# Optimization experiments

Measured on AMD Instinct MI355X. Metric: run time of the kernel, lower is better.

Reference implementation:

```python
import jax, jax.numpy as jnp
import numpy as np

D_MODEL = 5120
NUM_HEADS = 128
HEAD_DIM = D_MODEL // NUM_HEADS  # 40
LATENT = 1536


def setup_inputs() -> dict:
    key = jax.random.key(0)
    ks = jax.random.split(key, 9)
    B, S = 2, 1024
    scale = 0.02
    return {
        "x": jax.random.normal(ks[0], (B, S, D_MODEL), dtype=jnp.float32),
        "Wq": jax.random.normal(ks[1], (D_MODEL, D_MODEL), dtype=jnp.float32) * scale,
        "bq": jnp.zeros((D_MODEL,), dtype=jnp.float32),
        "Wc": jax.random.normal(ks[2], (D_MODEL, LATENT), dtype=jnp.float32) * scale,
        "bc": jnp.zeros((LATENT,), dtype=jnp.float32),
        "Wk": jax.random.normal(ks[3], (LATENT, D_MODEL), dtype=jnp.float32) * scale,
        "bk": jnp.zeros((D_MODEL,), dtype=jnp.float32),
        "Wv": jax.random.normal(ks[4], (LATENT, D_MODEL), dtype=jnp.float32) * scale,
        "bv": jnp.zeros((D_MODEL,), dtype=jnp.float32),
    }


def reference(x, Wq, bq, Wc, bc, Wk, bk, Wv, bv):
    B, S, _ = x.shape
    H, Dh = NUM_HEADS, HEAD_DIM
    # projections
    q = x @ Wq + bq                     # [B,S,D]
    kv_latent = x @ Wc + bc             # [B,S,L]
    k = kv_latent @ Wk + bk             # [B,S,D]
    v = kv_latent @ Wv + bv             # [B,S,D]
    # split heads -> [B,H,S,Dh]
    q = q.reshape(B, S, H, Dh).transpose(0, 2, 1, 3)
    k = k.reshape(B, S, H, Dh).transpose(0, 2, 1, 3)
    v = v.reshape(B, S, H, Dh).transpose(0, 2, 1, 3)
    scores = jnp.einsum("bhqd,bhkd->bhqk", q, k) / jnp.sqrt(jnp.float32(Dh))
    attn = jax.nn.softmax(scores, axis=-1)
    out = jnp.einsum("bhqk,bhkd->bhqd", attn, v)  # [B,H,S,Dh]
    return out.transpose(0, 2, 1, 3).reshape(B, S, H * Dh)
```

## Files before the change

kernel.cpp:

```cpp
#include <hip/hip_runtime.h>
#include <hip/hip_bf16.h>

typedef __attribute__((ext_vector_type(8))) __bf16 bf16x8;
typedef __attribute__((ext_vector_type(4))) __bf16 bf16x4;
typedef __attribute__((ext_vector_type(4))) float f32x4;

#define MFMA16(a, b, c) __builtin_amdgcn_mfma_f32_16x16x32_bf16((a), (b), (c), 0, 0, 0)

#if __has_builtin(__builtin_amdgcn_exp2f)
#define EXP2F(x) __builtin_amdgcn_exp2f(x)
#else
#define EXP2F(x) exp2f(x)
#endif

#define GLDS16(g, l)                                                             \
    __builtin_amdgcn_global_load_lds((const __attribute__((address_space(1))) void*)(g), \
                                     (__attribute__((address_space(3))) void*)(l), 16, 0, 0)

#define BARRIER()                          \
    do {                                   \
        asm volatile("" ::: "memory");     \
        __builtin_amdgcn_s_barrier();      \
        asm volatile("" ::: "memory");     \
    } while (0)

#define WAIT_LGKM0() asm volatile("s_waitcnt lgkmcnt(0)" ::: "memory")
#define VM6 asm volatile("s_waitcnt vmcnt(6)" ::: "memory")
#define VM8 asm volatile("s_waitcnt vmcnt(8)" ::: "memory")
#define VM0 asm volatile("s_waitcnt vmcnt(0)" ::: "memory")
#define VMNONE ((void)0)
#define KEEP(x) x
#define DROP(x)

static __device__ __forceinline__ unsigned short cvt_bf(float f) {
    return __builtin_bit_cast(unsigned short, (__bf16)f);
}

static __device__ __forceinline__ bf16x8 bf8_zero() {
    uint4 z = make_uint4(0, 0, 0, 0);
    return __builtin_bit_cast(bf16x8, z);
}

__global__ __launch_bounds__(256) void prep(const float* __restrict__ X,
                                            const float* __restrict__ Wq,
                                            const float* __restrict__ Wc,
                                            const float* __restrict__ Wk,
                                            const float* __restrict__ Wv,
                                            unsigned short* __restrict__ Xb,
                                            unsigned short* __restrict__ dqc,
                                            unsigned short* __restrict__ dkv) {
    const int D = 5120, L = 1536;
    int b = blockIdx.x, t = threadIdx.x;
    if (b < 5120) {
        int i = (b * 256 + t) * 8;
        float4 f0 = *(const float4*)(X + i);
        float4 f1 = *(const float4*)(X + i + 4);
        unsigned short o[8];
        o[0] = cvt_bf(f0.x); o[1] = cvt_bf(f0.y); o[2] = cvt_bf(f0.z); o[3] = cvt_bf(f0.w);
        o[4] = cvt_bf(f1.x); o[5] = cvt_bf(f1.y); o[6] = cvt_bf(f1.z); o[7] = cvt_bf(f1.w);
        *(uint4*)(Xb + i) = *(const uint4*)o;
        return;
    }
    int b2 = b - 5120;
    const float* W;
    unsigned short* WT;
    int K, N;
    if (b2 < 6400) { W = Wq; WT = dqc; K = D; N = D; }
    else if (b2 < 8320) { b2 -= 6400; W = Wc; WT = dqc + (size_t)D * D; K = D; N = L; }
    else if (b2 < 10240) { b2 -= 8320; W = Wk; WT = dkv; K = L; N = D; }
    else { b2 -= 10240; W = Wv; WT = dkv + (size_t)D * L; K = L; N = D; }
    int nx = N / 64;
    int n0 = (b2 % nx) * 64, k0 = (b2 / nx) * 64;

    __shared__ unsigned short tile[64][65];
    int c4 = (t & 15) * 4, r16 = t >> 4;
#pragma unroll
    for (int it = 0; it < 4; ++it) {
        int r = r16 + it * 16;
        float4 f = *(const float4*)&W[(size_t)(k0 + r) * N + n0 + c4];
        tile[r][c4 + 0] = cvt_bf(f.x);
        tile[r][c4 + 1] = cvt_bf(f.y);
        tile[r][c4 + 2] = cvt_bf(f.z);
        tile[r][c4 + 3] = cvt_bf(f.w);
    }
    __syncthreads();
    int n = t >> 2, kc = (t & 3) * 16;
    unsigned short o[16];
#pragma unroll
    for (int j = 0; j < 16; ++j) o[j] = tile[kc + j][n];
    unsigned short* dst = &WT[(size_t)(n0 + n) * K + k0 + kc];
    *(uint4*)dst = *(const uint4*)o;
    *(uint4*)(dst + 8) = *(const uint4*)(o + 8);
}

#define STAGE_A(S, H, KT)                                                              \
    do {                                                                               \
        GLDS16(aS[H][0] + (size_t)(KT) * 64, &Abuf[S][(H) * 8192 + wid * 512]);        \
        GLDS16(aS[H][1] + (size_t)(KT) * 64, &Abuf[S][(H) * 8192 + 4096 + wid * 512]); \
    } while (0)
#define STAGE_B(S, H, KT)                                                              \
    do {                                                                               \
        GLDS16(bS[H][0] + (size_t)(KT) * 64, &Bbuf[S][(H) * 8192 + wid * 512]);        \
        GLDS16(bS[H][1] + (size_t)(KT) * 64, &Bbuf[S][(H) * 8192 + 4096 + wid * 512]); \
    } while (0)

#define LDA_HALF(S, QM)                                                                   \
    do {                                                                                  \
        _Pragma("unroll") for (int mi = 0; mi < 4; ++mi)                                  \
            _Pragma("unroll") for (int kh = 0; kh < 2; ++kh)                              \
                af[mi][kh] =                                                              \
                    *(const bf16x8*)&Abuf[S][((QM) * 8192 + aoff + mi * 1024) ^ (kh * 32)]; \
    } while (0)
#define LDB_HALF(S, QN, BF)                                                               \
    do {                                                                                  \
        _Pragma("unroll") for (int ni = 0; ni < 2; ++ni)                                  \
            _Pragma("unroll") for (int kh = 0; kh < 2; ++kh)                              \
                BF[ni][kh] =                                                              \
                    *(const bf16x8*)&Bbuf[S][((QN) * 8192 + boff + ni * 1024) ^ (kh * 32)]; \
    } while (0)

#define MMAQ(QM, QN, BF)                                                                \
    do {                                                                                \
        _Pragma("unroll") for (int mi = 0; mi < 4; ++mi)                                \
            _Pragma("unroll") for (int ni = 0; ni < 2; ++ni)                            \
                _Pragma("unroll") for (int kh = 0; kh < 2; ++kh)                        \
                    acc[(QM) * 4 + mi][(QN) * 2 + ni] =                                 \
                        MFMA16(af[mi][kh], BF[ni][kh], acc[(QM) * 4 + mi][(QN) * 2 + ni]); \
    } while (0)

#define KTILE_V2(S, T, STG1, STG2, VMOP, RDNEXT)       \
    {                                                  \
        const int s_ = (S);                            \
        LDB_HALF(s_, 1, bf1);                          \
        STG1(STAGE_B(s_ ^ 1, 0, (T) + 1);)             \
        __builtin_amdgcn_s_setprio(1);                 \
        MMAQ(0, 0, bf0);                               \
        __builtin_amdgcn_s_setprio(0);                 \
        WAIT_LGKM0();                                  \
        BARRIER();                                     \
        STG2(STAGE_A(s_, 0, (T) + 2);                  \
             STAGE_B(s_, 1, (T) + 2);)                 \
        __builtin_amdgcn_s_setprio(1);                 \
        MMAQ(0, 1, bf1);                               \
        __builtin_amdgcn_s_setprio(0);                 \
        LDA_HALF(s_, 1);                               \
        __builtin_amdgcn_s_setprio(1);                 \
        MMAQ(1, 1, bf1);                               \
        __builtin_amdgcn_s_setprio(0);                 \
        WAIT_LGKM0();                                  \
        BARRIER();                                     \
        STG2(STAGE_A(s_, 1, (T) + 2);)                 \
        __builtin_amdgcn_s_setprio(1);                 \
        MMAQ(1, 0, bf0);                               \
        __builtin_amdgcn_s_setprio(0);                 \
        VMOP;                                          \
        BARRIER();                                     \
        RDNEXT(LDA_HALF(s_ ^ 1, 0); LDB_HALF(s_ ^ 1, 0, bf0);) \
    }

__global__ __launch_bounds__(512, 2) void gemm256(const unsigned short* __restrict__ A, int lda,
                                                  const unsigned short* __restrict__ BT, int ldb,
                                                  const float* __restrict__ bias0,
                                                  const float* __restrict__ bias1, int nsplit,
                                                  unsigned short* __restrict__ C, int ldc,
                                                  int K, float s0, float s1, int gx) {
    __shared__ __align__(16) unsigned short Abuf[2][16384];
    __shared__ __align__(16) unsigned short Bbuf[2][16384];

    int nwg = gridDim.x, orig = blockIdx.x;
    int cpx = nwg >> 3;
    int wgid = (orig & 7) * cpx + (orig >> 3);
    int tm = wgid / gx, tn = wgid % gx;
    int m0 = tm * 256, n0 = tn * 256;

    int tid = threadIdx.x, lane = tid & 63, wid = tid >> 6;
    int wm = wid >> 2, wn = wid & 3;
    int lrow = lane & 15, lkg = lane >> 4;

    int t5 = tid >> 3;
    int cole = ((tid & 7) ^ ((tid >> 3) & 7)) << 3;
    const unsigned short* aS[2][2];
    const unsigned short* bS[2][2];
#pragma unroll
    for (int H = 0; H < 2; ++H)
#pragma unroll
        for (int c = 0; c < 2; ++c) {
            int rA = (c << 7) | (H << 6) | t5;
            int rB = (((c << 1) | (t5 >> 5)) << 6) | (H << 5) | (t5 & 31);
            aS[H][c] = A + (size_t)(m0 + rA) * lda + cole;
            bS[H][c] = BT + (size_t)(n0 + rB) * ldb + cole;
        }

    int xorc = (lkg * 8) ^ ((lrow & 7) << 3);
    int aoff = wm * 4096 + lrow * 64 + xorc;
    int boff = wn * 2048 + lrow * 64 + xorc;

    f32x4 acc[8][4];
#pragma unroll
    for (int i = 0; i < 8; ++i)
#pragma unroll
        for (int j = 0; j < 4; ++j) acc[i][j] = (f32x4){0.f, 0.f, 0.f, 0.f};
    bf16x8 af[4][2], bf0[2][2], bf1[2][2];

    const int nkt = K >> 6;

    STAGE_A(0, 0, 0); STAGE_A(0, 1, 0); STAGE_B(0, 0, 0); STAGE_B(0, 1, 0);
    STAGE_A(1, 0, 1); STAGE_B(1, 1, 1); STAGE_A(1, 1, 1);
    VM6;
    BARRIER();
    LDA_HALF(0, 0);
    LDB_HALF(0, 0, bf0);

    int t = 0;
    for (; t + 2 < nkt; ++t) KTILE_V2(t & 1, t, KEEP, KEEP, VM6, KEEP);
    KTILE_V2(t & 1, t, KEEP, DROP, VM0, KEEP);
    ++t;
    KTILE_V2(t & 1, t, DROP, DROP, VMNONE, DROP);

#pragma unroll
    for (int ni = 0; ni < 4; ++ni) {
        int col = n0 + wn * 64 + ni * 16 + lrow;
        float bval = (col < nsplit) ? bias0[col] : bias1[col - nsplit];
        float scl = (col < nsplit) ? s0 : s1;
#pragma unroll
        for (int mi = 0; mi < 8; ++mi) {
            int row = m0 + wm * 128 + mi * 16 + lkg * 4;
#pragma unroll
            for (int j = 0; j < 4; ++j)
                C[(size_t)(row + j) * ldc + col] = cvt_bf((acc[mi][ni][j] + bval) * scl);
        }
    }
}

#define STG128(S, KT)                                                                  \
    do {                                                                               \
        _Pragma("unroll") for (int i_ = 0; i_ < 4; ++i_)                               \
            GLDS16(Ag + (size_t)(i_ * 32) * lda + (size_t)(KT) * 64,                   \
                   &Abuf[S][i_ * 2048 + wid * 512]);                                   \
        _Pragma("unroll") for (int i_ = 0; i_ < 4; ++i_)                               \
            GLDS16(Bg + (size_t)(i_ * 32) * ldb + (size_t)(KT) * 64,                   \
                   &Bbuf[S][i_ * 2048 + wid * 512]);                                   \
    } while (0)

__global__ __launch_bounds__(256, 2) void gemm128(const unsigned short* __restrict__ A, int lda,
                                                  const unsigned short* __restrict__ BT, int ldb,
                                                  const float* __restrict__ bias0,
                                                  const float* __restrict__ bias1, int nsplit,
                                                  unsigned short* __restrict__ C, int ldc,
                                                  unsigned short* __restrict__ VT,
                                                  int K, int gy) {
    __shared__ __align__(16) unsigned short Abuf[2][8192];
    __shared__ __align__(16) unsigned short Bbuf[2][8192];

    int b = blockIdx.x;
    int wgid = (b & 7) * (gridDim.x >> 3) + (b >> 3);
    int tm = wgid % gy, tn = wgid / gy;
    int m0 = tm * 128, n0 = tn * 128;
    int tid = threadIdx.x, lane = tid & 63, wid = tid >> 6;
    int wm = wid >> 1, wn = wid & 1;
    int lrow = lane & 15, lkg = lane >> 4;

    int srow = tid >> 3;
    int cole = ((tid & 7) ^ ((tid >> 3) & 7)) << 3;
    const unsigned short* Ag = A + (size_t)(m0 + srow) * lda + cole;
    const unsigned short* Bg = BT + (size_t)(n0 + srow) * ldb + cole;

    int xorc8 = (lrow & 7) << 3;
    int aoff = (wm * 64 + lrow) * 64;
    int boff = (wn * 64 + lrow) * 64;

    f32x4 acc[4][4];
#pragma unroll
    for (int i2 = 0; i2 < 4; ++i2)
#pragma unroll
        for (int j = 0; j < 4; ++j) acc[i2][j] = (f32x4){0.f, 0.f, 0.f, 0.f};

    const int nkt = K >> 6;
    STG128(0, 0);
    for (int t = 0; t < nkt; ++t) {
        const int cur = t & 1;
        if (t + 1 < nkt) {
            STG128(cur ^ 1, t + 1);
            VM8;
        } else {
            VM0;
        }
        BARRIER();
        bf16x8 af[4][2], bv[4][2];
#pragma unroll
        for (int mi = 0; mi < 4; ++mi)
#pragma unroll
            for (int kh = 0; kh < 2; ++kh)
                af[mi][kh] = *(const bf16x8*)&Abuf[cur][aoff + mi * 1024 + (((kh * 4 + lkg) << 3) ^ xorc8)];
#pragma unroll
        for (int ni = 0; ni < 4; ++ni)
#pragma unroll
            for (int kh = 0; kh < 2; ++kh)
                bv[ni][kh] = *(const bf16x8*)&Bbuf[cur][boff + ni * 1024 + (((kh * 4 + lkg) << 3) ^ xorc8)];
        __builtin_amdgcn_s_setprio(1);
#pragma unroll
        for (int mi = 0; mi < 4; ++mi)
#pragma unroll
            for (int ni = 0; ni < 4; ++ni)
#pragma unroll
                for (int kh = 0; kh < 2; ++kh)
                    acc[mi][ni] = MFMA16(af[mi][kh], bv[ni][kh], acc[mi][ni]);
        __builtin_amdgcn_s_setprio(0);
        BARRIER();
    }

#pragma unroll
    for (int ni = 0; ni < 4; ++ni) {
        int col = n0 + wn * 64 + ni * 16 + lrow;
        float bval = (col < nsplit) ? bias0[col] : bias1[col - nsplit];
#pragma unroll
        for (int mi = 0; mi < 4; ++mi) {
            int row = m0 + wm * 64 + mi * 16 + lkg * 4;
            if (col < nsplit) {
#pragma unroll
                for (int j = 0; j < 4; ++j)
                    C[(size_t)(row + j) * ldc + col] = cvt_bf(acc[mi][ni][j] + bval);
            } else {
                ushort4 o;
                o.x = cvt_bf(acc[mi][ni][0] + bval);
                o.y = cvt_bf(acc[mi][ni][1] + bval);
                o.z = cvt_bf(acc[mi][ni][2] + bval);
                o.w = cvt_bf(acc[mi][ni][3] + bval);
                *(ushort4*)&VT[(size_t)(col - nsplit) * 2048 + row] = o;
            }
        }
    }
}

__global__ __launch_bounds__(512) void attn(const unsigned short* __restrict__ q, int ldq,
                                            const unsigned short* __restrict__ k, int ldk,
                                            const unsigned short* __restrict__ vT,
                                            float* __restrict__ out) {
    const int S = 1024, D = 5120, Dh = 40;
    int b = blockIdx.z, h = blockIdx.y, qt = blockIdx.x;
    int t = threadIdx.x, lane = t & 63, wid = t >> 6;
    int lrow = lane & 15, lkg = lane >> 4;

    __shared__ __align__(16) unsigned short Ks[64 * 72];
    __shared__ __align__(16) unsigned short Vs[48 * 72];
    __shared__ __align__(16) unsigned short Ps[8][16 * 72];

    const size_t qbase = ((size_t)b * S) * ldq + (size_t)h * Dh;
    int q0 = qt * 256 + wid * 32;

    for (int z = t; z < 8 * 72; z += 512) Vs[40 * 72 + z] = 0;

    bf16x8 qf[2][2];
#pragma unroll
    for (int g = 0; g < 2; ++g) {
        const unsigned short* qp = q + qbase + (size_t)(q0 + g * 16 + lrow) * ldq;
        qf[g][0] = *(const bf16x8*)(qp + lkg * 8);
        qf[g][1] = (lkg == 0) ? *(const bf16x8*)(qp + 32) : bf8_zero();
    }

    int rrK = t >> 3, ccK = t & 7;
    int dV = t >> 3, cV = t & 7;
    int dVc = (dV < 40) ? dV : 39;
    const unsigned short* kp = k + ((size_t)b * S) * ldk + (size_t)h * Dh +
                               (size_t)rrK * ldk + ccK * 8;
    const unsigned short* vp = vT + (size_t)(h * Dh + dVc) * 2048 + b * S + cV * 8;
    const size_t kstep = (size_t)64 * ldk;

    uint4 kv0 = make_uint4(0, 0, 0, 0), va0 = make_uint4(0, 0, 0, 0);
    if (ccK < 5) kv0 = *(const uint4*)kp;
    if (dV < 40) va0 = *(const uint4*)vp;
    kp += kstep; vp += 64;

    f32x4 acc[2][3];
#pragma unroll
    for (int g = 0; g < 2; ++g)
#pragma unroll
        for (int nb = 0; nb < 3; ++nb) acc[g][nb] = (f32x4){0.f, 0.f, 0.f, 0.f};
    float mrun[2] = {-INFINITY, -INFINITY}, lrun[2] = {0.f, 0.f};

    for (int kt = 0; kt < 16; ++kt) {
        __syncthreads();
        uint4 w0 = (ccK < 5) ? kv0 : make_uint4(0, 0, 0, 0);
        *(uint4*)&Ks[rrK * 72 + ccK * 8] = w0;
        if (dV < 40) *(uint4*)&Vs[dV * 72 + cV * 8] = va0;
        __syncthreads();
        if (kt + 1 < 16) {
            if (ccK < 5) kv0 = *(const uint4*)kp;
            if (dV < 40) va0 = *(const uint4*)vp;
            kp += kstep; vp += 64;
        }

#pragma unroll
        for (int g = 0; g < 2; ++g) {
            f32x4 sf[4];
            __builtin_amdgcn_s_setprio(1);
#pragma unroll
            for (int nb = 0; nb < 4; ++nb) {
                sf[nb] = (f32x4){0.f, 0.f, 0.f, 0.f};
                bf16x8 kf0 = *(const bf16x8*)&Ks[(nb * 16 + lrow) * 72 + lkg * 8];
                bf16x8 kf1 = *(const bf16x8*)&Ks[(nb * 16 + lrow) * 72 + 32 + lkg * 8];
                sf[nb] = MFMA16(kf0, qf[g][0], sf[nb]);
                sf[nb] = MFMA16(kf1, qf[g][1], sf[nb]);
            }
            __builtin_amdgcn_s_setprio(0);

            float tm = sf[0][0];
#pragma unroll
            for (int nb = 0; nb < 4; ++nb)
#pragma unroll
                for (int i = 0; i < 4; ++i) tm = fmaxf(tm, sf[nb][i]);
            tm = fmaxf(tm, __shfl_xor(tm, 16));
            tm = fmaxf(tm, __shfl_xor(tm, 32));

            float mn = mrun[g], al = 1.0f;
            bool resc = !__all(tm <= mrun[g] + 11.0f);
            if (resc) {
                mn = fmaxf(mrun[g], tm);
                al = EXP2F(mrun[g] - mn);
                mrun[g] = mn;
            }
            float rs = 0.f;
#pragma unroll
            for (int nb = 0; nb < 4; ++nb) {
                bf16x4 pk;
#pragma unroll
                for (int i = 0; i < 4; ++i) {
                    float p = EXP2F(sf[nb][i] - mn);
                    rs += p;
                    pk[i] = (__bf16)p;
                }
                *(bf16x4*)&Ps[wid][lrow * 72 + nb * 16 + lkg * 4] = pk;
            }
            rs += __shfl_xor(rs, 16);
            rs += __shfl_xor(rs, 32);
            lrun[g] = lrun[g] * al + rs;

            if (resc) {
                float alr[4];
#pragma unroll
                for (int i = 0; i < 4; ++i) alr[i] = __shfl(al, lkg * 4 + i);
#pragma unroll
                for (int nb = 0; nb < 3; ++nb)
#pragma unroll
                    for (int i = 0; i < 4; ++i) acc[g][nb][i] *= alr[i];
            }

            __builtin_amdgcn_s_setprio(1);
#pragma unroll
            for (int kk = 0; kk < 2; ++kk) {
                bf16x8 pf = *(const bf16x8*)&Ps[wid][lrow * 72 + kk * 32 + lkg * 8];
#pragma unroll
                for (int nb = 0; nb < 3; ++nb) {
                    bf16x8 vf = *(const bf16x8*)&Vs[(nb * 16 + lrow) * 72 + kk * 32 + lkg * 8];
                    acc[g][nb] = MFMA16(pf, vf, acc[g][nb]);
                }
            }
            __builtin_amdgcn_s_setprio(0);
        }
    }

#pragma unroll
    for (int g = 0; g < 2; ++g) {
        float lr[4];
#pragma unroll
        for (int i = 0; i < 4; ++i) lr[i] = __shfl(lrun[g], lkg * 4 + i);
#pragma unroll
        for (int i = 0; i < 4; ++i) {
            float inv = 1.0f / lr[i];
            int s = q0 + g * 16 + lkg * 4 + i;
#pragma unroll
            for (int nb = 0; nb < 3; ++nb) {
                int d = nb * 16 + lrow;
                if (d < Dh) out[((size_t)(b * S + s)) * D + h * Dh + d] = acc[g][nb][i] * inv;
            }
        }
    }
}

extern "C" void kernel_launch(void* const* d_in, const int* in_sizes, int n_in,
                              void* d_out, int out_size, void* d_ws, size_t ws_size,
                              hipStream_t stream) {
    const int M = 2048, D = 5120, L = 1536, NQ = D + L , NKV = 2 * D ;
    const float* x  = (const float*)d_in[0];
    const float* Wq = (const float*)d_in[1];
    const float* bq = (const float*)d_in[2];
    const float* Wc = (const float*)d_in[3];
    const float* bc = (const float*)d_in[4];
    const float* Wk = (const float*)d_in[5];
    const float* bk = (const float*)d_in[6];
    const float* Wv = (const float*)d_in[7];
    const float* bv = (const float*)d_in[8];
    float* out = (float*)d_out;

    unsigned short* ws = (unsigned short*)d_ws;
    size_t off = 0;
    unsigned short* xb    = ws + off; off += (size_t)M * D;
    unsigned short* WqcT  = ws + off; off += (size_t)NQ * D;
    unsigned short* WkvT  = ws + off; off += (size_t)NKV * L;
    unsigned short* qkvb  = ws + off; off += (size_t)M * NQ;
    unsigned short* kvout = ws + off; off += (size_t)M * NKV;
    unsigned short* vTb   = ws + off; off += (size_t)D * M;

    prep<<<17280, 256, 0, stream>>>(x, Wq, Wc, Wk, Wv, xb, WqcT, WkvT);

    const float qscale = 1.4426950408889634f / 6.324555320336759f;

    gemm256<<<dim3((NQ / 256) * (M / 256)), 512, 0, stream>>>(xb, D, WqcT, D, bq, bc, D,
                                                              qkvb, NQ, D, qscale, 1.0f,
                                                              NQ / 256);
    gemm128<<<dim3((NKV / 128) * (M / 128)), 256, 0, stream>>>(qkvb + D, NQ, WkvT, L, bk, bv, D,
                                                               kvout, NKV, vTb, L, M / 128);

    attn<<<dim3(1024 / 256, 128, 2), 512, 0, stream>>>(qkvb, NQ, kvout, NKV, vTb, out);
}
```

Measured before the change: 437.7 us.

## Replace 256x256 Q/latent GEMM with generic 128x128 GEMM kernel

Removes the specialized 256x256-tile, 512-thread GEMM with its hand-scheduled split pipeline and runs the first projection (x times [Wq|Wc]) through the existing 128x128 GEMM instead. The 128 kernel gains per-column scale arguments and a null VT path so it can write the scaled Q output directly. The smaller tiles give more workgroups and simpler scheduling, at the cost of lower operand reuse per loaded tile for the large M=2048, N=6656, K=5120 GEMM.

Result: slower. 459.6 us (+5.0%).

```diff
diff --git a/kernel.cpp b/kernel.cpp
--- a/kernel.cpp
+++ b/kernel.cpp
@@ -24,13 +24,8 @@
         asm volatile("" ::: "memory");     \
     } while (0)
 
-#define WAIT_LGKM0() asm volatile("s_waitcnt lgkmcnt(0)" ::: "memory")
-#define VM6 asm volatile("s_waitcnt vmcnt(6)" ::: "memory")
 #define VM8 asm volatile("s_waitcnt vmcnt(8)" ::: "memory")
 #define VM0 asm volatile("s_waitcnt vmcnt(0)" ::: "memory")
-#define VMNONE ((void)0)
-#define KEEP(x) x
-#define DROP(x)
 
 static __device__ __forceinline__ unsigned short cvt_bf(float f) {
     return __builtin_bit_cast(unsigned short, (__bf16)f);
@@ -93,145 +88,6 @@
     *(uint4*)(dst + 8) = *(const uint4*)(o + 8);
 }
 
-#define STAGE_A(S, H, KT)                                                              \
-    do {                                                                               \
-        GLDS16(aS[H][0] + (size_t)(KT) * 64, &Abuf[S][(H) * 8192 + wid * 512]);        \
-        GLDS16(aS[H][1] + (size_t)(KT) * 64, &Abuf[S][(H) * 8192 + 4096 + wid * 512]); \
-    } while (0)
-#define STAGE_B(S, H, KT)                                                              \
-    do {                                                                               \
-        GLDS16(bS[H][0] + (size_t)(KT) * 64, &Bbuf[S][(H) * 8192 + wid * 512]);        \
-        GLDS16(bS[H][1] + (size_t)(KT) * 64, &Bbuf[S][(H) * 8192 + 4096 + wid * 512]); \
-    } while (0)
-
-#define LDA_HALF(S, QM)                                                                   \
-    do {                                                                                  \
-        _Pragma("unroll") for (int mi = 0; mi < 4; ++mi)                                  \
-            _Pragma("unroll") for (int kh = 0; kh < 2; ++kh)                              \
-                af[mi][kh] =                                                              \
-                    *(const bf16x8*)&Abuf[S][((QM) * 8192 + aoff + mi * 1024) ^ (kh * 32)]; \
-    } while (0)
-#define LDB_HALF(S, QN, BF)                                                               \
-    do {                                                                                  \
-        _Pragma("unroll") for (int ni = 0; ni < 2; ++ni)                                  \
-            _Pragma("unroll") for (int kh = 0; kh < 2; ++kh)                              \
-                BF[ni][kh] =                                                              \
-                    *(const bf16x8*)&Bbuf[S][((QN) * 8192 + boff + ni * 1024) ^ (kh * 32)]; \
-    } while (0)
-
-#define MMAQ(QM, QN, BF)                                                                \
-    do {                                                                                \
-        _Pragma("unroll") for (int mi = 0; mi < 4; ++mi)                                \
-            _Pragma("unroll") for (int ni = 0; ni < 2; ++ni)                            \
-                _Pragma("unroll") for (int kh = 0; kh < 2; ++kh)                        \
-                    acc[(QM) * 4 + mi][(QN) * 2 + ni] =                                 \
-                        MFMA16(af[mi][kh], BF[ni][kh], acc[(QM) * 4 + mi][(QN) * 2 + ni]); \
-    } while (0)
-
-#define KTILE_V2(S, T, STG1, STG2, VMOP, RDNEXT)       \
-    {                                                  \
-        const int s_ = (S);                            \
-        LDB_HALF(s_, 1, bf1);                          \
-        STG1(STAGE_B(s_ ^ 1, 0, (T) + 1);)             \
-        __builtin_amdgcn_s_setprio(1);                 \
-        MMAQ(0, 0, bf0);                               \
-        __builtin_amdgcn_s_setprio(0);                 \
-        WAIT_LGKM0();                                  \
-        BARRIER();                                     \
-        STG2(STAGE_A(s_, 0, (T) + 2);                  \
-             STAGE_B(s_, 1, (T) + 2);)                 \
-        __builtin_amdgcn_s_setprio(1);                 \
-        MMAQ(0, 1, bf1);                               \
-        __builtin_amdgcn_s_setprio(0);                 \
-        LDA_HALF(s_, 1);                               \
-        __builtin_amdgcn_s_setprio(1);                 \
-        MMAQ(1, 1, bf1);                               \
-        __builtin_amdgcn_s_setprio(0);                 \
-        WAIT_LGKM0();                                  \
-        BARRIER();                                     \
-        STG2(STAGE_A(s_, 1, (T) + 2);)                 \
-        __builtin_amdgcn_s_setprio(1);                 \
-        MMAQ(1, 0, bf0);                               \
-        __builtin_amdgcn_s_setprio(0);                 \
-        VMOP;                                          \
-        BARRIER();                                     \
-        RDNEXT(LDA_HALF(s_ ^ 1, 0); LDB_HALF(s_ ^ 1, 0, bf0);) \
-    }
-
-__global__ __launch_bounds__(512, 2) void gemm256(const unsigned short* __restrict__ A, int lda,
-                                                  const unsigned short* __restrict__ BT, int ldb,
-                                                  const float* __restrict__ bias0,
-                                                  const float* __restrict__ bias1, int nsplit,
-                                                  unsigned short* __restrict__ C, int ldc,
-                                                  int K, float s0, float s1, int gx) {
-    __shared__ __align__(16) unsigned short Abuf[2][16384];
-    __shared__ __align__(16) unsigned short Bbuf[2][16384];
-
-    int nwg = gridDim.x, orig = blockIdx.x;
-    int cpx = nwg >> 3;
-    int wgid = (orig & 7) * cpx + (orig >> 3);
-    int tm = wgid / gx, tn = wgid % gx;
-    int m0 = tm * 256, n0 = tn * 256;
-
-    int tid = threadIdx.x, lane = tid & 63, wid = tid >> 6;
-    int wm = wid >> 2, wn = wid & 3;
-    int lrow = lane & 15, lkg = lane >> 4;
-
-    int t5 = tid >> 3;
-    int cole = ((tid & 7) ^ ((tid >> 3) & 7)) << 3;
-    const unsigned short* aS[2][2];
-    const unsigned short* bS[2][2];
-#pragma unroll
-    for (int H = 0; H < 2; ++H)
-#pragma unroll
-        for (int c = 0; c < 2; ++c) {
-            int rA = (c << 7) | (H << 6) | t5;
-            int rB = (((c << 1) | (t5 >> 5)) << 6) | (H << 5) | (t5 & 31);
-            aS[H][c] = A + (size_t)(m0 + rA) * lda + cole;
-            bS[H][c] = BT + (size_t)(n0 + rB) * ldb + cole;
-        }
-
-    int xorc = (lkg * 8) ^ ((lrow & 7) << 3);
-    int aoff = wm * 4096 + lrow * 64 + xorc;
-    int boff = wn * 2048 + lrow * 64 + xorc;
-
-    f32x4 acc[8][4];
-#pragma unroll
-    for (int i = 0; i < 8; ++i)
-#pragma unroll
-        for (int j = 0; j < 4; ++j) acc[i][j] = (f32x4){0.f, 0.f, 0.f, 0.f};
-    bf16x8 af[4][2], bf0[2][2], bf1[2][2];
-
-    const int nkt = K >> 6;
-
-    STAGE_A(0, 0, 0); STAGE_A(0, 1, 0); STAGE_B(0, 0, 0); STAGE_B(0, 1, 0);
-    STAGE_A(1, 0, 1); STAGE_B(1, 1, 1); STAGE_A(1, 1, 1);
-    VM6;
-    BARRIER();
-    LDA_HALF(0, 0);
-    LDB_HALF(0, 0, bf0);
-
-    int t = 0;
-    for (; t + 2 < nkt; ++t) KTILE_V2(t & 1, t, KEEP, KEEP, VM6, KEEP);
-    KTILE_V2(t & 1, t, KEEP, DROP, VM0, KEEP);
-    ++t;
-    KTILE_V2(t & 1, t, DROP, DROP, VMNONE, DROP);
-
-#pragma unroll
-    for (int ni = 0; ni < 4; ++ni) {
-        int col = n0 + wn * 64 + ni * 16 + lrow;
-        float bval = (col < nsplit) ? bias0[col] : bias1[col - nsplit];
-        float scl = (col < nsplit) ? s0 : s1;
-#pragma unroll
-        for (int mi = 0; mi < 8; ++mi) {
-            int row = m0 + wm * 128 + mi * 16 + lkg * 4;
-#pragma unroll
-            for (int j = 0; j < 4; ++j)
-                C[(size_t)(row + j) * ldc + col] = cvt_bf((acc[mi][ni][j] + bval) * scl);
-        }
-    }
-}
-
 #define STG128(S, KT)                                                                  \
     do {                                                                               \
         _Pragma("unroll") for (int i_ = 0; i_ < 4; ++i_)                               \
@@ -248,7 +104,7 @@
                                                   const float* __restrict__ bias1, int nsplit,
                                                   unsigned short* __restrict__ C, int ldc,
                                                   unsigned short* __restrict__ VT,
-                                                  int K, int gy) {
+                                                  int K, float s0, float s1, int gy) {
     __shared__ __align__(16) unsigned short Abuf[2][8192];
     __shared__ __align__(16) unsigned short Bbuf[2][8192];
 
@@ -313,13 +169,14 @@
     for (int ni = 0; ni < 4; ++ni) {
         int col = n0 + wn * 64 + ni * 16 + lrow;
         float bval = (col < nsplit) ? bias0[col] : bias1[col - nsplit];
+        float scl = (col < nsplit) ? s0 : s1;
 #pragma unroll
         for (int mi = 0; mi < 4; ++mi) {
             int row = m0 + wm * 64 + mi * 16 + lkg * 4;
-            if (col < nsplit) {
+            if (VT == nullptr || col < nsplit) {
 #pragma unroll
                 for (int j = 0; j < 4; ++j)
-                    C[(size_t)(row + j) * ldc + col] = cvt_bf(acc[mi][ni][j] + bval);
+                    C[(size_t)(row + j) * ldc + col] = cvt_bf((acc[mi][ni][j] + bval) * scl);
             } else {
                 ushort4 o;
                 o.x = cvt_bf(acc[mi][ni][0] + bval);
@@ -505,11 +362,12 @@
 
     const float qscale = 1.4426950408889634f / 6.324555320336759f;
 
-    gemm256<<<dim3((NQ / 256) * (M / 256)), 512, 0, stream>>>(xb, D, WqcT, D, bq, bc, D,
-                                                              qkvb, NQ, D, qscale, 1.0f,
-                                                              NQ / 256);
+    gemm128<<<dim3((NQ / 128) * (M / 128)), 256, 0, stream>>>(xb, D, WqcT, D, bq, bc, D,
+                                                              qkvb, NQ, (unsigned short*)nullptr,
+                                                              D, qscale, 1.0f, M / 128);
     gemm128<<<dim3((NKV / 128) * (M / 128)), 256, 0, stream>>>(qkvb + D, NQ, WkvT, L, bk, bv, D,
-                                                               kvout, NKV, vTb, L, M / 128);
+                                                               kvout, NKV, vTb, L, 1.0f, 1.0f,
+                                                               M / 128);
 
     attn<<<dim3(1024 / 256, 128, 2), 512, 0, stream>>>(qkvb, NQ, kvout, NKV, vTb, out);
 }
```
